# Kernel optimization log

Hardware: AMD Instinct MI355X
Metric: run time of the kernel (lower is better)

Reference implementation:

```python
import jax, jax.numpy as jnp
import numpy as np
from jax import lax


def conv2d(x, w, stride=1, padding=0, dilation=1, bias=None):
    s = (stride, stride) if isinstance(stride, int) else stride
    p = (padding, padding) if isinstance(padding, int) else padding
    d = (dilation, dilation) if isinstance(dilation, int) else dilation
    out = lax.conv_general_dilated(x, w, s, [(p[0], p[0]), (p[1], p[1])],
                                   rhs_dilation=d,
                                   dimension_numbers=('NCHW', 'OIHW', 'NCHW'))
    if bias is not None:
        out = out + bias[None, :, None, None]
    return out


def bn(x, eps=1e-5):
    # BatchNorm2d in training mode with default affine params (gamma=1, beta=0)
    m = x.mean((0, 2, 3), keepdims=True)
    v = jnp.mean((x - m) ** 2, (0, 2, 3), keepdims=True)
    return (x - m) * lax.rsqrt(v + eps)


def cbam(x, w_fc1, w_fc2, w_sp):
    mlp = lambda v: conv2d(jax.nn.relu(conv2d(v, w_fc1)), w_fc2)
    ca = jax.nn.sigmoid(mlp(x.mean((2, 3), keepdims=True)) + mlp(x.max((2, 3), keepdims=True)))
    x = x * ca
    sp = jnp.concatenate([x.mean(1, keepdims=True), x.max(1, keepdims=True)], 1)
    return x * jax.nn.sigmoid(conv2d(sp, w_sp, padding=3))


def deform_conv(x, offset, w_kernel, ks=3, padding=1):
    b, c, h, w = x.shape
    N = ks * ks
    # reorder interleaved offsets -> all x-offsets then all y-offsets
    reorder = jnp.concatenate([jnp.arange(0, 2 * N, 2), jnp.arange(1, 2 * N, 2)])
    offset = offset[:, reorder]
    xp = jnp.pad(x, ((0, 0), (0, 0), (padding, padding), (padding, padding)))
    Hp, Wp = h + 2 * padding, w + 2 * padding
    r = jnp.arange(-(ks - 1) // 2, (ks - 1) // 2 + 1)
    knx, kny = jnp.meshgrid(r, r, indexing='ij')
    p_n = jnp.concatenate([knx.ravel(), kny.ravel()]).astype(x.dtype).reshape(1, 2 * N, 1, 1)
    gx, gy = jnp.meshgrid(jnp.arange(1, h + 1), jnp.arange(1, w + 1), indexing='ij')
    p_0 = jnp.concatenate([jnp.broadcast_to(gx[None, None], (1, N, h, w)),
                           jnp.broadcast_to(gy[None, None], (1, N, h, w))], 1).astype(x.dtype)
    p = jnp.transpose(p_0 + p_n + offset, (0, 2, 3, 1))  # [b,h,w,2N]
    clampq = lambda q: jnp.concatenate([jnp.clip(q[..., :N], 0, Hp - 1),
                                        jnp.clip(q[..., N:], 0, Wp - 1)], -1)
    fl = jnp.floor(lax.stop_gradient(p))
    q_lt = clampq(fl).astype(jnp.int32)
    q_rb = clampq(fl + 1).astype(jnp.int32)
    q_lb = jnp.concatenate([q_lt[..., :N], q_rb[..., N:]], -1)
    q_rt = jnp.concatenate([q_rb[..., :N], q_lt[..., N:]], -1)
    mask = jnp.concatenate([(p[..., :N] < padding) | (p[..., :N] > Hp - 1 - padding),
                            (p[..., N:] < padding) | (p[..., N:] > Wp - 1 - padding)], -1)
    mask = lax.stop_gradient(mask.astype(p.dtype))
    # floor_p = p - (p - floor(p)) carries zero gradient in the original
    p = p * (1 - mask) + lax.stop_gradient(jnp.floor(p)) * mask
    p = clampq(p)
    px, py = p[..., :N], p[..., N:]
    def g(q, sx, sy):
        return ((1 + sx * (q[..., :N].astype(p.dtype) - px)) *
                (1 + sy * (q[..., N:].astype(p.dtype) - py)))
    xf = xp.reshape(b, c, Hp * Wp)
    def gather(q):
        idx = (q[..., :N] * Wp + q[..., N:]).reshape(b, 1, h * w * N)
        v = jnp.take_along_axis(xf, jnp.broadcast_to(idx, (b, c, h * w * N)), axis=2)
        return v.reshape(b, c, h, w, N)
    xo = (g(q_lt, 1, 1)[:, None] * gather(q_lt) + g(q_rb, -1, -1)[:, None] * gather(q_rb)
          + g(q_lb, 1, -1)[:, None] * gather(q_lb) + g(q_rt, -1, 1)[:, None] * gather(q_rt))
    # [b,c,h,w,N] -> [b,c,h*ks,w*ks] (N = kernel_row*ks + kernel_col)
    xo = xo.reshape(b, c, h, w, ks, ks).transpose(0, 1, 2, 4, 3, 5).reshape(b, c, h * ks, w * ks)
    return conv2d(xo, w_kernel, stride=ks)


def _forward(lf, hf, w_conv1_1, b_conv1_1, w_conv, w_offset, b_offset, w_deform,
             w_dil1, w_dil2, w_dil3, w_dil4, w_conv1, w_conv2,
             w_fc1, w_fc2, w_sp, w_conv1_2, b_conv1_2, w_conv3_3):
    hf = jax.nn.relu(bn(conv2d(hf, w_conv1_1, bias=b_conv1_1)))  # Conv1x1
    xc = jnp.split(lf, 4, axis=1)
    def branch(prev, extra, w_dil, dil):
        x = bn(conv2d(jnp.concatenate([prev, hf], 1), w_conv, padding=1))
        t = x + extra
        off = conv2d(t, w_offset, padding=1, bias=b_offset)
        d = deform_conv(t, off, w_deform)
        d = bn(conv2d(d, w_dil, padding=dil, dilation=dil))
        d = bn(conv2d(d, w_conv1, padding=1))
        d = cbam(d, w_fc1, w_fc2, w_sp)
        return bn(conv2d(d, w_conv2, padding=1))
    x0_1 = branch(xc[0], xc[1], w_dil1, 1)
    x1_2 = branch(x0_1, x0_1 + xc[2], w_dil2, 2)
    x2_3 = branch(x1_2, x1_2 + xc[3], w_dil3, 3)
    x3_4 = branch(x2_3, x2_3, w_dil4, 4)
    xx = jax.nn.relu(bn(conv2d(jnp.concatenate([x0_1, x1_2, x2_3, x3_4], 1),
                               w_conv1_2, bias=b_conv1_2)))
    return bn(conv2d(lf + xx, w_conv3_3, padding=1))


def setup_inputs() -> dict:
    key = jax.random.key(0)
    ks = jax.random.split(key, 20)
    B, C, H, W = 4, 64, 256, 256
    c4 = C // 4
    rn = lambda k, shp, s=0.05: jax.random.normal(k, shp, dtype=jnp.float32) * s
    return {
        'lf': rn(ks[0], (B, C, H, W), 1.0),
        'hf': rn(ks[1], (B, C, H, W), 1.0),
        'w_conv1_1': rn(ks[2], (c4, C, 1, 1)),
        'b_conv1_1': jnp.zeros((c4,), jnp.float32),
        'w_conv': rn(ks[3], (c4, C // 2, 3, 3)),
        'w_offset': rn(ks[4], (18, c4, 3, 3)),
        'b_offset': jnp.zeros((18,), jnp.float32),
        'w_deform': rn(ks[5], (c4, c4, 3, 3)),
        'w_dil1': rn(ks[6], (c4, c4, 3, 3)),
        'w_dil2': rn(ks[7], (c4, c4, 3, 3)),
        'w_dil3': rn(ks[8], (c4, c4, 3, 3)),
        'w_dil4': rn(ks[9], (c4, c4, 3, 3)),
        'w_conv1': rn(ks[10], (C, c4, 3, 3)),
        'w_conv2': rn(ks[11], (c4, C, 3, 3)),
        'w_fc1': rn(ks[12], (C // 16, C, 1, 1)),
        'w_fc2': rn(ks[13], (C, C // 16, 1, 1)),
        'w_sp': rn(ks[14], (1, 2, 7, 7)),
        'w_conv1_2': rn(ks[15], (C, C, 1, 1)),
        'b_conv1_2': jnp.zeros((C,), jnp.float32),
        'w_conv3_3': rn(ks[16], (C, C, 3, 3)),
    }


def reference(lf, hf, w_conv1_1, b_conv1_1, w_conv, w_offset, b_offset, w_deform,
              w_dil1, w_dil2, w_dil3, w_dil4, w_conv1, w_conv2,
              w_fc1, w_fc2, w_sp, w_conv1_2, b_conv1_2, w_conv3_3):
    return _forward(lf, hf, w_conv1_1, b_conv1_1, w_conv, w_offset, b_offset, w_deform,
                    w_dil1, w_dil2, w_dil3, w_dil4, w_conv1, w_conv2,
                    w_fc1, w_fc2, w_sp, w_conv1_2, b_conv1_2, w_conv3_3)
```

## Files before the change

### kernel.cpp

```cpp
#include <hip/hip_runtime.h>
#include <math.h>

#define HW 65536
#define Wd 256
#define Hd 256
#define Bn 4
#define NS 16

template<int CIN1,int CIN2,int COUT,int COB,int DIL>
__global__ __launch_bounds__(256) void conv3_k(
    const float* __restrict__ inA, long long a_bs,
    const float* __restrict__ inB,
    const float* __restrict__ add_in,
    const float* __restrict__ w, const float* __restrict__ bias,
    const float* __restrict__ scale_c, const float* __restrict__ scale_p,
    float* __restrict__ out)
{
    constexpr int CIN = CIN1 + CIN2;
    constexpr int SP = 2*DIL + 4;
    int tx = threadIdx.x & 15, ty = threadIdx.x >> 4;
    int j0 = blockIdx.x*64 + tx*4;
    int iy = blockIdx.y & 15;
    int chunk = blockIdx.y >> 4;
    int i = iy*16 + ty;
    int b = blockIdx.z;
    int o0 = chunk*COB;

    float acc[COB][4];
#pragma unroll
    for(int o=0;o<COB;o++){
        float bv = bias ? bias[o0+o] : 0.f;
#pragma unroll
        for(int q=0;q<4;q++) acc[o][q] = bv;
    }

    const float* spb = scale_p ? scale_p + (size_t)b*HW : nullptr;

    for(int c=0;c<CIN;c++){
        const float* cb;
        if (CIN2 == 0 || c < CIN1) cb = inA + (size_t)b*a_bs + (size_t)c*HW;
        else                       cb = inB + ((size_t)b*CIN2 + (c-CIN1))*HW;
        const float* ab = add_in ? add_in + (size_t)b*a_bs + (size_t)c*HW : nullptr;
        float sc = scale_c ? scale_c[b*CIN + c] : 1.f;

        float r[3][SP];
#pragma unroll
        for(int kh=0;kh<3;kh++){
#pragma unroll
            for(int t=0;t<SP;t++) r[kh][t] = 0.f;
            int ii = i + (kh-1)*DIL;
            if (ii < 0 || ii >= Hd) continue;
            const float* row = cb + ii*Wd;
            float4 c4 = *(const float4*)(row + j0);
            r[kh][DIL+0]=c4.x; r[kh][DIL+1]=c4.y; r[kh][DIL+2]=c4.z; r[kh][DIL+3]=c4.w;
#pragma unroll
            for(int t=0;t<DIL;t++){
                int jl = j0 - DIL + t;
                if (jl >= 0) r[kh][t] = row[jl];
                int jr = j0 + 4 + t;
                if (jr < Wd) r[kh][DIL+4+t] = row[jr];
            }
            if (ab){
                const float* arow = ab + ii*Wd;
                float4 a4 = *(const float4*)(arow + j0);
                r[kh][DIL+0]+=a4.x; r[kh][DIL+1]+=a4.y; r[kh][DIL+2]+=a4.z; r[kh][DIL+3]+=a4.w;
#pragma unroll
                for(int t=0;t<DIL;t++){
                    int jl = j0 - DIL + t;
                    if (jl >= 0) r[kh][t] += arow[jl];
                    int jr = j0 + 4 + t;
                    if (jr < Wd) r[kh][DIL+4+t] += arow[jr];
                }
            }
            if (spb){
                const float* srow = spb + ii*Wd;
                float4 s4 = *(const float4*)(srow + j0);
                r[kh][DIL+0]*=s4.x; r[kh][DIL+1]*=s4.y; r[kh][DIL+2]*=s4.z; r[kh][DIL+3]*=s4.w;
#pragma unroll
                for(int t=0;t<DIL;t++){
                    int jl = j0 - DIL + t;
                    if (jl >= 0) r[kh][t] *= srow[jl];
                    int jr = j0 + 4 + t;
                    if (jr < Wd) r[kh][DIL+4+t] *= srow[jr];
                }
            }
            if (scale_c){
#pragma unroll
                for(int t=0;t<SP;t++) r[kh][t] *= sc;
            }
        }

#pragma unroll
        for(int o=0;o<COB;o++){
#pragma unroll
            for(int kh=0;kh<3;kh++){
#pragma unroll
                for(int kw=0;kw<3;kw++){
                    float ww = w[((size_t)(o0+o)*CIN + c)*9 + kh*3 + kw];
#pragma unroll
                    for(int q=0;q<4;q++)
                        acc[o][q] = fmaf(ww, r[kh][kw*DIL + q], acc[o][q]);
                }
            }
        }
    }

    float* ob = out + ((size_t)b*COUT + o0)*HW + i*Wd + j0;
#pragma unroll
    for(int o=0;o<COB;o++){
        float4 v; v.x=acc[o][0]; v.y=acc[o][1]; v.z=acc[o][2]; v.w=acc[o][3];
        *(float4*)(ob + (size_t)o*HW) = v;
    }
}

template<int CIN,int COUT>
__global__ void conv1x1_k(const float* __restrict__ in, const float* __restrict__ w,
                          const float* __restrict__ bias, float* __restrict__ out)
{
    int p = blockIdx.x*256 + threadIdx.x;
    int b = blockIdx.y;
    const float* inb = in + (size_t)b*CIN*HW + p;
    float acc[COUT];
#pragma unroll
    for(int o=0;o<COUT;o++) acc[o] = bias ? bias[o] : 0.f;
    for(int c=0;c<CIN;c++){
        float v = inb[(size_t)c*HW];
#pragma unroll
        for(int o=0;o<COUT;o++) acc[o] += w[o*CIN+c]*v;
    }
    float* ob = out + (size_t)b*COUT*HW + p;
#pragma unroll
    for(int o=0;o<COUT;o++) ob[(size_t)o*HW] = acc[o];
}

__global__ void bn_stats_part(const float* __restrict__ x, int C, double* __restrict__ part)
{
    int c = blockIdx.x, s = blockIdx.y, tid = threadIdx.x;
    double sum = 0.0, sum2 = 0.0;
    for(int t=0;t<64;t++){
        int g = s*16384 + t*256 + tid;
        int b = g >> 16, p = g & 65535;
        double v = (double)x[((size_t)b*C + c)*HW + p];
        sum += v; sum2 += v*v;
    }
    __shared__ double sh[512];
    sh[tid] = sum; sh[256+tid] = sum2;
    __syncthreads();
    for(int o=128;o>0;o>>=1){
        if (tid < o){ sh[tid] += sh[tid+o]; sh[256+tid] += sh[256+tid+o]; }
        __syncthreads();
    }
    if (tid==0){ part[(c*NS+s)*2] = sh[0]; part[(c*NS+s)*2+1] = sh[256]; }
}

__global__ void bn_finalize(const double* __restrict__ part, int C, float* __restrict__ mr)
{
    int c = threadIdx.x;
    if (c >= C) return;
    double s = 0.0, s2 = 0.0;
    for(int k=0;k<NS;k++){ s += part[(c*NS+k)*2]; s2 += part[(c*NS+k)*2+1]; }
    double n = (double)Bn*HW;
    double m = s/n;
    double var = s2/n - m*m;
    mr[c]   = (float)m;
    mr[C+c] = rsqrtf((float)var + 1e-5f);
}

__global__ void bn_apply_k(const float* __restrict__ x, const float* __restrict__ mr, int C,
                           const float* __restrict__ e1, long long e1_bs,
                           const float* __restrict__ e2, long long e2_bs,
                           float* __restrict__ out, int relu)
{
    int p = (blockIdx.x*256 + threadIdx.x)*4;
    int c = blockIdx.y, b = blockIdx.z;
    size_t idx = ((size_t)b*C + c)*HW + p;
    float m = mr[c], r = mr[C+c];
    float4 v = *(const float4*)(x + idx);
    v.x = (v.x-m)*r; v.y = (v.y-m)*r; v.z = (v.z-m)*r; v.w = (v.w-m)*r;
    if (e1){
        float4 a = *(const float4*)(e1 + (size_t)b*e1_bs + (size_t)c*HW + p);
        v.x+=a.x; v.y+=a.y; v.z+=a.z; v.w+=a.w;
    }
    if (e2){
        float4 a = *(const float4*)(e2 + (size_t)b*e2_bs + (size_t)c*HW + p);
        v.x+=a.x; v.y+=a.y; v.z+=a.z; v.w+=a.w;
    }
    if (relu){
        v.x=fmaxf(v.x,0.f); v.y=fmaxf(v.y,0.f); v.z=fmaxf(v.z,0.f); v.w=fmaxf(v.w,0.f);
    }
    *(float4*)(out + idx) = v;
}

__global__ void cat4_k(const float* __restrict__ x0, const float* __restrict__ x1,
                       const float* __restrict__ x2, const float* __restrict__ x3,
                       float* __restrict__ out)
{
    int p = (blockIdx.x*256 + threadIdx.x)*4;
    int c = blockIdx.y, b = blockIdx.z;
    const float* src = (c<16)? x0 : (c<32)? x1 : (c<48)? x2 : x3;
    *(float4*)(out + ((size_t)b*64 + c)*HW + p) =
        *(const float4*)(src + ((size_t)b*16 + (c&15))*HW + p);
}

__global__ void deform_k(const float* __restrict__ t, const float* __restrict__ off,
                         const float* __restrict__ w, float* __restrict__ out)
{
    int tx = threadIdx.x & 15, ty = threadIdx.x >> 4;
    int j = blockIdx.x*16 + tx;
    int i = blockIdx.y*16 + ty;
    int b = blockIdx.z;
    const float* tb = t + (size_t)b*16*HW;
    const float* ob = off + (size_t)b*18*HW + i*Wd + j;
    float acc[16];
#pragma unroll
    for(int o=0;o<16;o++) acc[o] = 0.f;

    for(int n=0;n<9;n++){
        float offx = ob[(size_t)(2*n)*HW];
        float offy = ob[(size_t)(2*n+1)*HW];
        float px = (float)(i + n/3) + offx;
        float py = (float)(j + n%3) + offy;
        float flx = floorf(px), fly = floorf(py);
        float qltx = fminf(fmaxf(flx,       0.f), 257.f);
        float qlty = fminf(fmaxf(fly,       0.f), 257.f);
        float qrbx = fminf(fmaxf(flx + 1.f, 0.f), 257.f);
        float qrby = fminf(fmaxf(fly + 1.f, 0.f), 257.f);
        if (px < 1.f || px > 256.f) px = flx;
        if (py < 1.f || py > 256.f) py = fly;
        px = fminf(fmaxf(px, 0.f), 257.f);
        py = fminf(fmaxf(py, 0.f), 257.f);
        float wx_lt = 1.f + (qltx - px);
        float wx_rb = 1.f - (qrbx - px);
        float wy_lt = 1.f + (qlty - py);
        float wy_rb = 1.f - (qrby - py);
        float glt = wx_lt*wy_lt, grb = wx_rb*wy_rb, glb = wx_lt*wy_rb, grt = wx_rb*wy_lt;
        int ix0 = (int)qltx - 1, iy0 = (int)qlty - 1;
        int ix1 = (int)qrbx - 1, iy1 = (int)qrby - 1;
        bool vx0 = (ix0>=0 && ix0<Hd), vx1 = (ix1>=0 && ix1<Hd);
        bool vy0 = (iy0>=0 && iy0<Wd), vy1 = (iy1>=0 && iy1<Wd);
        int i00 = ix0*Wd+iy0, i01 = ix0*Wd+iy1, i10 = ix1*Wd+iy0, i11 = ix1*Wd+iy1;
        float vals[16];
#pragma unroll
        for(int c=0;c<16;c++){
            const float* tc = tb + (size_t)c*HW;
            float v00 = (vx0&&vy0) ? tc[i00] : 0.f;
            float v11 = (vx1&&vy1) ? tc[i11] : 0.f;
            float v01 = (vx0&&vy1) ? tc[i01] : 0.f;
            float v10 = (vx1&&vy0) ? tc[i10] : 0.f;
            vals[c] = glt*v00 + grb*v11 + glb*v01 + grt*v10;
        }
#pragma unroll
        for(int o=0;o<16;o++){
            float a = acc[o];
#pragma unroll
            for(int c=0;c<16;c++) a += w[(o*16+c)*9 + n] * vals[c];
            acc[o] = a;
        }
    }
    float* outb = out + (size_t)b*16*HW + i*Wd + j;
#pragma unroll
    for(int o=0;o<16;o++) outb[(size_t)o*HW] = acc[o];
}

__global__ void pool_k(const float* __restrict__ x, float* __restrict__ pavg, float* __restrict__ pmax)
{
    int bc = blockIdx.x;
    int tid = threadIdx.x;
    const float* p = x + (size_t)bc*HW;
    float s = 0.f, mx = -1e30f;
    for(int i=tid;i<HW;i+=256){ float v = p[i]; s += v; mx = fmaxf(mx, v); }
    __shared__ float sh[512];
    sh[tid] = s; sh[256+tid] = mx;
    __syncthreads();
    for(int o=128;o>0;o>>=1){
        if (tid < o){ sh[tid] += sh[tid+o]; sh[256+tid] = fmaxf(sh[256+tid], sh[256+tid+o]); }
        __syncthreads();
    }
    if (tid==0){ pavg[bc] = sh[0] / (float)HW; pmax[bc] = sh[256]; }
}

__global__ void ca_k(const float* __restrict__ pavg, const float* __restrict__ pmax,
                     const float* __restrict__ w1, const float* __restrict__ w2,
                     float* __restrict__ ca)
{
    int b = blockIdx.x;
    int tid = threadIdx.x;
    __shared__ float ha[4], hm[4];
    if (tid < 4){
        float sa = 0.f, sm = 0.f;
        for(int c=0;c<64;c++){
            sa += w1[tid*64+c] * pavg[b*64+c];
            sm += w1[tid*64+c] * pmax[b*64+c];
        }
        ha[tid] = fmaxf(sa, 0.f);
        hm[tid] = fmaxf(sm, 0.f);
    }
    __syncthreads();
    float s = 0.f;
    for(int h=0;h<4;h++) s += w2[tid*4+h] * (ha[h] + hm[h]);
    ca[b*64+tid] = 1.f / (1.f + expf(-s));
}

__global__ void spstats_k(const float* __restrict__ x, const float* __restrict__ ca,
                          float* __restrict__ spm, float* __restrict__ spx)
{
    int p = blockIdx.x*256 + threadIdx.x;
    int b = blockIdx.y;
    const float* xb = x + (size_t)b*64*HW + p;
    const float* cb = ca + b*64;
    float s = 0.f, mx = -1e30f;
    for(int c=0;c<64;c++){
        float v = xb[(size_t)c*HW] * cb[c];
        s += v; mx = fmaxf(mx, v);
    }
    spm[(size_t)b*HW+p] = s * (1.f/64.f);
    spx[(size_t)b*HW+p] = mx;
}

__global__ void spconv_k(const float* __restrict__ spm, const float* __restrict__ spx,
                         const float* __restrict__ wsp, float* __restrict__ sa)
{
    int tx = threadIdx.x & 15, ty = threadIdx.x >> 4;
    int j = blockIdx.x*16 + tx;
    int i = blockIdx.y*16 + ty;
    int b = blockIdx.z;
    const float* m = spm + (size_t)b*HW;
    const float* x = spx + (size_t)b*HW;
    float s = 0.f;
    for(int kh=0;kh<7;kh++){
        int ii = i + kh - 3; if (ii<0||ii>=Hd) continue;
        for(int kw=0;kw<7;kw++){
            int jj = j + kw - 3; if (jj<0||jj>=Wd) continue;
            s += wsp[kh*7+kw]*m[ii*Wd+jj] + wsp[49+kh*7+kw]*x[ii*Wd+jj];
        }
    }
    sa[(size_t)b*HW + i*Wd + j] = 1.f / (1.f + expf(-s));
}

extern "C" void kernel_launch(void* const* d_in, const int* in_sizes, int n_in,
                              void* d_out, int out_size, void* d_ws, size_t ws_size,
                              hipStream_t stream)
{
    const float* lf        = (const float*)d_in[0];
    const float* hf        = (const float*)d_in[1];
    const float* w_conv1_1 = (const float*)d_in[2];
    const float* b_conv1_1 = (const float*)d_in[3];
    const float* w_conv    = (const float*)d_in[4];
    const float* w_offset  = (const float*)d_in[5];
    const float* b_offset  = (const float*)d_in[6];
    const float* w_deform  = (const float*)d_in[7];
    const float* w_dil[4]  = {(const float*)d_in[8],(const float*)d_in[9],
                              (const float*)d_in[10],(const float*)d_in[11]};
    const float* w_conv1   = (const float*)d_in[12];
    const float* w_conv2   = (const float*)d_in[13];
    const float* w_fc1     = (const float*)d_in[14];
    const float* w_fc2     = (const float*)d_in[15];
    const float* w_sp      = (const float*)d_in[16];
    const float* w_conv1_2 = (const float*)d_in[17];
    const float* b_conv1_2 = (const float*)d_in[18];
    const float* w_conv3_3 = (const float*)d_in[19];
    float* out = (float*)d_out;

    float* ws = (float*)d_ws;
    size_t off_f = 0;
    auto alloc = [&](size_t n){ float* p = ws + off_f; off_f += n; return p; };
    const size_t S16 = (size_t)Bn*16*HW;

    float* hf_p  = alloc(S16);
    float* B16_0 = alloc(S16);
    float* B16_1 = alloc(S16);
    float* B16_2 = alloc(S16);
    float* B64F  = ws;
    float* Boff  = alloc((size_t)Bn*18*HW);
    float* B64_0 = alloc((size_t)Bn*64*HW);
    float* xk[4] = {alloc(S16),alloc(S16),alloc(S16),alloc(S16)};
    float* spm   = alloc((size_t)Bn*HW);
    float* spx   = alloc((size_t)Bn*HW);
    float* sa    = alloc((size_t)Bn*HW);
    float* mr    = alloc(128);
    float* pavg  = alloc(256);
    float* pmax  = alloc(256);
    float* ca    = alloc(256);
    double* part = (double*)alloc(64*NS*2*2);
    (void)ws_size; (void)in_sizes; (void)n_in; (void)out_size;

    dim3 blk(256);
    dim3 gpix(HW/256, Bn);
    dim3 gtile(16,16,Bn);
    dim3 gapply16(HW/1024,16,Bn), gapply64(HW/1024,64,Bn);
    const long long bs16 = 16LL*HW, bs64 = 64LL*HW;

    auto bn_stats = [&](const float* x, int C){
        bn_stats_part<<<dim3(C,NS),blk,0,stream>>>(x, C, part);
        bn_finalize<<<1,64,0,stream>>>(part, C, mr);
    };

    conv1x1_k<64,16><<<gpix,blk,0,stream>>>(hf, w_conv1_1, b_conv1_1, hf_p);
    bn_stats(hf_p, 16);
    bn_apply_k<<<gapply16,blk,0,stream>>>(hf_p, mr, 16, nullptr,0, nullptr,0, hf_p, 1);

    for(int k=0;k<4;k++){
        const float* prev; long long prev_bs;
        if (k==0){ prev = lf;      prev_bs = bs64; }
        else     { prev = xk[k-1]; prev_bs = bs16; }
        conv3_k<16,16,16,16,1><<<dim3(4,16,Bn),blk,0,stream>>>(
            prev, prev_bs, hf_p, nullptr, w_conv, nullptr, nullptr, nullptr, B16_0);
        bn_stats(B16_0, 16);
        const float* e1; long long e1bs; const float* e2 = nullptr; long long e2bs = 0;
        if (k==0){ e1 = lf + 16*HW; e1bs = bs64; }
        else if (k==3){ e1 = xk[2]; e1bs = bs16; }
        else { e1 = xk[k-1]; e1bs = bs16; e2 = lf + (size_t)(k+1)*16*HW; e2bs = bs64; }
        bn_apply_k<<<gapply16,blk,0,stream>>>(B16_0, mr, 16, e1,e1bs, e2,e2bs, B16_0, 0);
        conv3_k<16,0,18,18,1><<<dim3(4,16,Bn),blk,0,stream>>>(
            B16_0, bs16, nullptr, nullptr, w_offset, b_offset, nullptr, nullptr, Boff);
        deform_k<<<gtile,blk,0,stream>>>(B16_0, Boff, w_deform, B16_1);
        switch(k){
        case 0: conv3_k<16,0,16,16,1><<<dim3(4,16,Bn),blk,0,stream>>>(B16_1, bs16, nullptr, nullptr, w_dil[0], nullptr, nullptr, nullptr, B16_2); break;
        case 1: conv3_k<16,0,16,16,2><<<dim3(4,16,Bn),blk,0,stream>>>(B16_1, bs16, nullptr, nullptr, w_dil[1], nullptr, nullptr, nullptr, B16_2); break;
        case 2: conv3_k<16,0,16,16,3><<<dim3(4,16,Bn),blk,0,stream>>>(B16_1, bs16, nullptr, nullptr, w_dil[2], nullptr, nullptr, nullptr, B16_2); break;
        case 3: conv3_k<16,0,16,16,4><<<dim3(4,16,Bn),blk,0,stream>>>(B16_1, bs16, nullptr, nullptr, w_dil[3], nullptr, nullptr, nullptr, B16_2); break;
        }
        bn_stats(B16_2, 16);
        bn_apply_k<<<gapply16,blk,0,stream>>>(B16_2, mr, 16, nullptr,0, nullptr,0, B16_2, 0);
        conv3_k<16,0,64,16,1><<<dim3(4,64,Bn),blk,0,stream>>>(
            B16_2, bs16, nullptr, nullptr, w_conv1, nullptr, nullptr, nullptr, B64_0);
        bn_stats(B64_0, 64);
        bn_apply_k<<<gapply64,blk,0,stream>>>(B64_0, mr, 64, nullptr,0, nullptr,0, B64_0, 0);
        pool_k<<<Bn*64,blk,0,stream>>>(B64_0, pavg, pmax);
        ca_k<<<Bn,dim3(64),0,stream>>>(pavg, pmax, w_fc1, w_fc2, ca);
        spstats_k<<<dim3(256,Bn),blk,0,stream>>>(B64_0, ca, spm, spx);
        spconv_k<<<gtile,blk,0,stream>>>(spm, spx, w_sp, sa);
        conv3_k<64,0,16,16,1><<<dim3(4,16,Bn),blk,0,stream>>>(
            B64_0, bs64, nullptr, nullptr, w_conv2, nullptr, ca, sa, B16_1);
        bn_stats(B16_1, 16);
        bn_apply_k<<<gapply16,blk,0,stream>>>(B16_1, mr, 16, nullptr,0, nullptr,0, xk[k], 0);
    }

    cat4_k<<<dim3(HW/1024,64,Bn),blk,0,stream>>>(xk[0], xk[1], xk[2], xk[3], B64F);
    conv1x1_k<64,64><<<gpix,blk,0,stream>>>(B64F, w_conv1_2, b_conv1_2, B64_0);
    bn_stats(B64_0, 64);
    bn_apply_k<<<gapply64,blk,0,stream>>>(B64_0, mr, 64, nullptr,0, nullptr,0, B64_0, 1);
    conv3_k<64,0,64,16,1><<<dim3(4,64,Bn),blk,0,stream>>>(
        lf, bs64, nullptr, B64_0, w_conv3_3, nullptr, nullptr, nullptr, B64F);
    bn_stats(B64F, 64);
    bn_apply_k<<<gapply64,blk,0,stream>>>(B64F, mr, 64, nullptr,0, nullptr,0, out, 0);
}
```

Measured before the change: 4.327 ms.

## Fuse BatchNorm statistics into conv epilogues via atomics and halve output-channel blocking

```diff
diff --git a/kernel.cpp b/kernel.cpp
--- a/kernel.cpp
+++ b/kernel.cpp
@@ -5,7 +5,14 @@
 #define Wd 256
 #define Hd 256
 #define Bn 4
-#define NS 16
+
+__device__ __forceinline__ void atomAddF(float* p, float v){
+    __hip_atomic_fetch_add(p, v, __ATOMIC_RELAXED, __HIP_MEMORY_SCOPE_AGENT);
+}
+
+__global__ void zero_k(float* __restrict__ p, int n){
+    for(int i = blockIdx.x*256 + threadIdx.x; i < n; i += gridDim.x*256) p[i] = 0.f;
+}
 
 template<int CIN1,int CIN2,int COUT,int COB,int DIL>
 __global__ __launch_bounds__(256) void conv3_k(
@@ -14,7 +21,7 @@
     const float* __restrict__ add_in,
     const float* __restrict__ w, const float* __restrict__ bias,
     const float* __restrict__ scale_c, const float* __restrict__ scale_p,
-    float* __restrict__ out)
+    float* __restrict__ out, float* __restrict__ stats)
 {
     constexpr int CIN = CIN1 + CIN2;
     constexpr int SP = 2*DIL + 4;
@@ -111,11 +118,31 @@
         float4 v; v.x=acc[o][0]; v.y=acc[o][1]; v.z=acc[o][2]; v.w=acc[o][3];
         *(float4*)(ob + (size_t)o*HW) = v;
     }
+
+    if (stats){
+#pragma unroll
+        for(int o=0;o<COB;o++){
+            float s  = acc[o][0]+acc[o][1]+acc[o][2]+acc[o][3];
+            float s2 = acc[o][0]*acc[o][0]+acc[o][1]*acc[o][1]
+                     + acc[o][2]*acc[o][2]+acc[o][3]*acc[o][3];
+#pragma unroll
+            for(int d=32;d>0;d>>=1){
+                s  += __shfl_down(s,  d, 64);
+                s2 += __shfl_down(s2, d, 64);
+            }
+            if ((threadIdx.x & 63) == 0){
+                float* pc = stats + (size_t)(o0+o)*8 + ((threadIdx.x>>6)&3);
+                atomAddF(pc,   s);
+                atomAddF(pc+4, s2);
+            }
+        }
+    }
 }
 
 template<int CIN,int COUT>
 __global__ void conv1x1_k(const float* __restrict__ in, const float* __restrict__ w,
-                          const float* __restrict__ bias, float* __restrict__ out)
+                          const float* __restrict__ bias, float* __restrict__ out,
+                          float* __restrict__ stats)
 {
     int p = blockIdx.x*256 + threadIdx.x;
     int b = blockIdx.y;
@@ -131,50 +158,39 @@
     float* ob = out + (size_t)b*COUT*HW + p;
 #pragma unroll
     for(int o=0;o<COUT;o++) ob[(size_t)o*HW] = acc[o];
-}
-
-__global__ void bn_stats_part(const float* __restrict__ x, int C, double* __restrict__ part)
-{
-    int c = blockIdx.x, s = blockIdx.y, tid = threadIdx.x;
-    double sum = 0.0, sum2 = 0.0;
-    for(int t=0;t<64;t++){
-        int g = s*16384 + t*256 + tid;
-        int b = g >> 16, p = g & 65535;
-        double v = (double)x[((size_t)b*C + c)*HW + p];
-        sum += v; sum2 += v*v;
-    }
-    __shared__ double sh[512];
-    sh[tid] = sum; sh[256+tid] = sum2;
-    __syncthreads();
-    for(int o=128;o>0;o>>=1){
-        if (tid < o){ sh[tid] += sh[tid+o]; sh[256+tid] += sh[256+tid+o]; }
-        __syncthreads();
-    }
-    if (tid==0){ part[(c*NS+s)*2] = sh[0]; part[(c*NS+s)*2+1] = sh[256]; }
-}
-
-__global__ void bn_finalize(const double* __restrict__ part, int C, float* __restrict__ mr)
-{
-    int c = threadIdx.x;
-    if (c >= C) return;
-    double s = 0.0, s2 = 0.0;
-    for(int k=0;k<NS;k++){ s += part[(c*NS+k)*2]; s2 += part[(c*NS+k)*2+1]; }
-    double n = (double)Bn*HW;
-    double m = s/n;
-    double var = s2/n - m*m;
-    mr[c]   = (float)m;
-    mr[C+c] = rsqrtf((float)var + 1e-5f);
-}
-
-__global__ void bn_apply_k(const float* __restrict__ x, const float* __restrict__ mr, int C,
+
+    if (stats){
+#pragma unroll
+        for(int o=0;o<COUT;o++){
+            float s = acc[o], s2 = acc[o]*acc[o];
+#pragma unroll
+            for(int d=32;d>0;d>>=1){
+                s  += __shfl_down(s,  d, 64);
+                s2 += __shfl_down(s2, d, 64);
+            }
+            if ((threadIdx.x & 63) == 0){
+                float* pc = stats + (size_t)o*8 + ((threadIdx.x>>6)&3);
+                atomAddF(pc,   s);
+                atomAddF(pc+4, s2);
+            }
+        }
+    }
+}
+
+__global__ void bn_apply_k(const float* __restrict__ x, const float* __restrict__ stats, int C,
                            const float* __restrict__ e1, long long e1_bs,
                            const float* __restrict__ e2, long long e2_bs,
                            float* __restrict__ out, int relu)
 {
     int p = (blockIdx.x*256 + threadIdx.x)*4;
     int c = blockIdx.y, b = blockIdx.z;
+    const float* pc = stats + (size_t)c*8;
+    float s  = pc[0]+pc[1]+pc[2]+pc[3];
+    float s2 = pc[4]+pc[5]+pc[6]+pc[7];
+    const float inv_n = 1.f / (float)((long long)Bn*HW);
+    float m = s*inv_n;
+    float r = rsqrtf(fmaxf(s2*inv_n - m*m, 0.f) + 1e-5f);
     size_t idx = ((size_t)b*C + c)*HW + p;
-    float m = mr[c], r = mr[C+c];
     float4 v = *(const float4*)(x + idx);
     v.x = (v.x-m)*r; v.y = (v.y-m)*r; v.z = (v.z-m)*r; v.w = (v.w-m)*r;
     if (e1){
@@ -377,71 +393,70 @@
     float* spm   = alloc((size_t)Bn*HW);
     float* spx   = alloc((size_t)Bn*HW);
     float* sa    = alloc((size_t)Bn*HW);
-    float* mr    = alloc(128);
     float* pavg  = alloc(256);
     float* pmax  = alloc(256);
     float* ca    = alloc(256);
-    double* part = (double*)alloc(64*NS*2*2);
+    float* stats = alloc(8192);
     (void)ws_size; (void)in_sizes; (void)n_in; (void)out_size;
+
+    int soff = 0;
+    auto salloc = [&](int C){ float* p = stats + soff; soff += C*8; return p; };
+    float* stA = salloc(16);
+    float *stT[4], *stD[4], *stC1[4], *stC2[4];
+    for(int k=0;k<4;k++){ stT[k]=salloc(16); stD[k]=salloc(16); stC1[k]=salloc(64); stC2[k]=salloc(16); }
+    float* stXX  = salloc(64);
+    float* stOut = salloc(64);
 
     dim3 blk(256);
     dim3 gpix(HW/256, Bn);
     dim3 gtile(16,16,Bn);
     dim3 gapply16(HW/1024,16,Bn), gapply64(HW/1024,64,Bn);
+    dim3 g16(4,32,Bn);
+    dim3 g64(4,128,Bn);
     const long long bs16 = 16LL*HW, bs64 = 64LL*HW;
 
-    auto bn_stats = [&](const float* x, int C){
-        bn_stats_part<<<dim3(C,NS),blk,0,stream>>>(x, C, part);
-        bn_finalize<<<1,64,0,stream>>>(part, C, mr);
-    };
-
-    conv1x1_k<64,16><<<gpix,blk,0,stream>>>(hf, w_conv1_1, b_conv1_1, hf_p);
-    bn_stats(hf_p, 16);
-    bn_apply_k<<<gapply16,blk,0,stream>>>(hf_p, mr, 16, nullptr,0, nullptr,0, hf_p, 1);
+    zero_k<<<dim3(8),blk,0,stream>>>(stats, soff);
+
+    conv1x1_k<64,16><<<gpix,blk,0,stream>>>(hf, w_conv1_1, b_conv1_1, hf_p, stA);
+    bn_apply_k<<<gapply16,blk,0,stream>>>(hf_p, stA, 16, nullptr,0, nullptr,0, hf_p, 1);
 
     for(int k=0;k<4;k++){
         const float* prev; long long prev_bs;
         if (k==0){ prev = lf;      prev_bs = bs64; }
         else     { prev = xk[k-1]; prev_bs = bs16; }
-        conv3_k<16,16,16,16,1><<<dim3(4,16,Bn),blk,0,stream>>>(
-            prev, prev_bs, hf_p, nullptr, w_conv, nullptr, nullptr, nullptr, B16_0);
-        bn_stats(B16_0, 16);
+        conv3_k<16,16,16,8,1><<<g16,blk,0,stream>>>(
+            prev, prev_bs, hf_p, nullptr, w_conv, nullptr, nullptr, nullptr, B16_0, stT[k]);
         const float* e1; long long e1bs; const float* e2 = nullptr; long long e2bs = 0;
         if (k==0){ e1 = lf + 16*HW; e1bs = bs64; }
         else if (k==3){ e1 = xk[2]; e1bs = bs16; }
         else { e1 = xk[k-1]; e1bs = bs16; e2 = lf + (size_t)(k+1)*16*HW; e2bs = bs64; }
-        bn_apply_k<<<gapply16,blk,0,stream>>>(B16_0, mr, 16, e1,e1bs, e2,e2bs, B16_0, 0);
-        conv3_k<16,0,18,18,1><<<dim3(4,16,Bn),blk,0,stream>>>(
-            B16_0, bs16, nullptr, nullptr, w_offset, b_offset, nullptr, nullptr, Boff);
+        bn_apply_k<<<gapply16,blk,0,stream>>>(B16_0, stT[k], 16, e1,e1bs, e2,e2bs, B16_0, 0);
+        conv3_k<16,0,18,9,1><<<g16,blk,0,stream>>>(
+            B16_0, bs16, nullptr, nullptr, w_offset, b_offset, nullptr, nullptr, Boff, nullptr);
         deform_k<<<gtile,blk,0,stream>>>(B16_0, Boff, w_deform, B16_1);
         switch(k){
-        case 0: conv3_k<16,0,16,16,1><<<dim3(4,16,Bn),blk,0,stream>>>(B16_1, bs16, nullptr, nullptr, w_dil[0], nullptr, nullptr, nullptr, B16_2); break;
-        case 1: conv3_k<16,0,16,16,2><<<dim3(4,16,Bn),blk,0,stream>>>(B16_1, bs16, nullptr, nullptr, w_dil[1], nullptr, nullptr, nullptr, B16_2); break;
-        case 2: conv3_k<16,0,16,16,3><<<dim3(4,16,Bn),blk,0,stream>>>(B16_1, bs16, nullptr, nullptr, w_dil[2], nullptr, nullptr, nullptr, B16_2); break;
-        case 3: conv3_k<16,0,16,16,4><<<dim3(4,16,Bn),blk,0,stream>>>(B16_1, bs16, nullptr, nullptr, w_dil[3], nullptr, nullptr, nullptr, B16_2); break;
-        }
-        bn_stats(B16_2, 16);
-        bn_apply_k<<<gapply16,blk,0,stream>>>(B16_2, mr, 16, nullptr,0, nullptr,0, B16_2, 0);
-        conv3_k<16,0,64,16,1><<<dim3(4,64,Bn),blk,0,stream>>>(
-            B16_2, bs16, nullptr, nullptr, w_conv1, nullptr, nullptr, nullptr, B64_0);
-        bn_stats(B64_0, 64);
-        bn_apply_k<<<gapply64,blk,0,stream>>>(B64_0, mr, 64, nullptr,0, nullptr,0, B64_0, 0);
+        case 0: conv3_k<16,0,16,8,1><<<g16,blk,0,stream>>>(B16_1, bs16, nullptr, nullptr, w_dil[0], nullptr, nullptr, nullptr, B16_2, stD[k]); break;
+        case 1: conv3_k<16,0,16,8,2><<<g16,blk,0,stream>>>(B16_1, bs16, nullptr, nullptr, w_dil[1], nullptr, nullptr, nullptr, B16_2, stD[k]); break;
+        case 2: conv3_k<16,0,16,8,3><<<g16,blk,0,stream>>>(B16_1, bs16, nullptr, nullptr, w_dil[2], nullptr, nullptr, nullptr, B16_2, stD[k]); break;
+        case 3: conv3_k<16,0,16,8,4><<<g16,blk,0,stream>>>(B16_1, bs16, nullptr, nullptr, w_dil[3], nullptr, nullptr, nullptr, B16_2, stD[k]); break;
+        }
+        bn_apply_k<<<gapply16,blk,0,stream>>>(B16_2, stD[k], 16, nullptr,0, nullptr,0, B16_2, 0);
+        conv3_k<16,0,64,8,1><<<g64,blk,0,stream>>>(
+            B16_2, bs16, nullptr, nullptr, w_conv1, nullptr, nullptr, nullptr, B64_0, stC1[k]);
+        bn_apply_k<<<gapply64,blk,0,stream>>>(B64_0, stC1[k], 64, nullptr,0, nullptr,0, B64_0, 0);
         pool_k<<<Bn*64,blk,0,stream>>>(B64_0, pavg, pmax);
         ca_k<<<Bn,dim3(64),0,stream>>>(pavg, pmax, w_fc1, w_fc2, ca);
         spstats_k<<<dim3(256,Bn),blk,0,stream>>>(B64_0, ca, spm, spx);
         spconv_k<<<gtile,blk,0,stream>>>(spm, spx, w_sp, sa);
-        conv3_k<64,0,16,16,1><<<dim3(4,16,Bn),blk,0,stream>>>(
-            B64_0, bs64, nullptr, nullptr, w_conv2, nullptr, ca, sa, B16_1);
-        bn_stats(B16_1, 16);
-        bn_apply_k<<<gapply16,blk,0,stream>>>(B16_1, mr, 16, nullptr,0, nullptr,0, xk[k], 0);
+        conv3_k<64,0,16,8,1><<<g16,blk,0,stream>>>(
+            B64_0, bs64, nullptr, nullptr, w_conv2, nullptr, ca, sa, B16_1, stC2[k]);
+        bn_apply_k<<<gapply16,blk,0,stream>>>(B16_1, stC2[k], 16, nullptr,0, nullptr,0, xk[k], 0);
     }
 
     cat4_k<<<dim3(HW/1024,64,Bn),blk,0,stream>>>(xk[0], xk[1], xk[2], xk[3], B64F);
-    conv1x1_k<64,64><<<gpix,blk,0,stream>>>(B64F, w_conv1_2, b_conv1_2, B64_0);
-    bn_stats(B64_0, 64);
-    bn_apply_k<<<gapply64,blk,0,stream>>>(B64_0, mr, 64, nullptr,0, nullptr,0, B64_0, 1);
-    conv3_k<64,0,64,16,1><<<dim3(4,64,Bn),blk,0,stream>>>(
-        lf, bs64, nullptr, B64_0, w_conv3_3, nullptr, nullptr, nullptr, B64F);
-    bn_stats(B64F, 64);
-    bn_apply_k<<<gapply64,blk,0,stream>>>(B64F, mr, 64, nullptr,0, nullptr,0, out, 0);
-}
+    conv1x1_k<64,64><<<gpix,blk,0,stream>>>(B64F, w_conv1_2, b_conv1_2, B64_0, stXX);
+    bn_apply_k<<<gapply64,blk,0,stream>>>(B64_0, stXX, 64, nullptr,0, nullptr,0, B64_0, 1);
+    conv3_k<64,0,64,8,1><<<g64,blk,0,stream>>>(
+        lf, bs64, nullptr, B64_0, w_conv3_3, nullptr, nullptr, nullptr, B64F, stOut);
+    bn_apply_k<<<gapply64,blk,0,stream>>>(B64F, stOut, 64, nullptr,0, nullptr,0, out, 0);
+}
```

Measured after the change: 6.352 ms. 46.8% more time.
